# Kernel tuning notes

Hardware: AMD Instinct MI355X
Metric: run time of the kernel (lower is better)

The kernel has to match this reference:

```python
import jax, jax.numpy as jnp
import numpy as np
from jax import lax

B, T, S, J, D = 8, 512, 32, 64, 400
R, MDU, TAGS = 256, 100, 7


def _lstm(x, Wih, Whh, bih, bhh):
    """PyTorch-convention LSTM over x [N,L,Din]; gate order i,f,g,o.
    Returns (hs, cs) each [N,L,R] in scan order (not re-flipped)."""
    N = x.shape[0]
    Rh = Whh.shape[1]
    h0 = jnp.zeros((N, Rh), x.dtype)
    xW = x @ Wih.T + (bih + bhh)  # precompute input projection [N,L,4R]

    def step(carry, xt):
        h, c = carry
        g = xt + h @ Whh.T
        i, f, gg, o = jnp.split(g, 4, axis=-1)
        c = jax.nn.sigmoid(f) * c + jax.nn.sigmoid(i) * jnp.tanh(gg)
        h = jax.nn.sigmoid(o) * jnp.tanh(c)
        return (h, c), (h, c)

    _, (hs, cs) = lax.scan(step, (h0, h0), xW.transpose(1, 0, 2))
    return hs.transpose(1, 0, 2), cs.transpose(1, 0, 2)


def setup_inputs() -> dict:
    key = jax.random.key(0)
    ks = jax.random.split(key, 40)

    def rn(i, shape, s=0.1):
        return s * jax.random.normal(ks[i], shape, jnp.float32)

    inp = {
        'input_text': rn(0, (B, T, D), 1.0),
        'input_syn': rn(1, (B, S, J, D), 1.0),
        'label': jax.random.randint(ks[2], (B, T), 0, TAGS),
        'len_context': jnp.full((B,), T, jnp.int32),
        'len_synopsis': jnp.full((B, S), J, jnp.int32),
    }
    # 6 LSTM parameter sets: context f1/b1 (in=D), synopsis f/b (in=D), modeling f/b (in=4R)
    idx = 3
    for name, din in [('f1', D), ('b1', D), ('sf', D), ('sb', D), ('mf', 4 * R), ('mb', 4 * R)]:
        inp['Wih_' + name] = rn(idx, (4 * R, din)); idx += 1
        inp['Whh_' + name] = rn(idx, (4 * R, R)); idx += 1
        inp['bih_' + name] = rn(idx, (4 * R,)); idx += 1
        inp['bhh_' + name] = rn(idx, (4 * R,)); idx += 1
    inp['W_cWh'] = rn(idx, (MDU, 2 * R)); idx += 1
    inp['W_cWu'] = rn(idx, (MDU, 2 * R)); idx += 1
    inp['W_v'] = rn(idx, (1, MDU)); idx += 1
    inp['W_sWh'] = rn(idx, (2 * R, 2 * R)); idx += 1
    inp['W_sWu'] = rn(idx, (2 * R, 2 * R)); idx += 1
    inp['W_Ws'] = rn(idx, (MDU, 2 * R)); idx += 1
    inp['W_out'] = rn(idx, (TAGS, 6 * R)); idx += 1
    inp['b_out'] = rn(idx, (TAGS,)); idx += 1
    return inp


def reference(input_text, input_syn, label, len_context, len_synopsis,
              Wih_f1, Whh_f1, bih_f1, bhh_f1,
              Wih_b1, Whh_b1, bih_b1, bhh_b1,
              Wih_sf, Whh_sf, bih_sf, bhh_sf,
              Wih_sb, Whh_sb, bih_sb, bhh_sb,
              Wih_mf, Whh_mf, bih_mf, bhh_mf,
              Wih_mb, Whh_mb, bih_mb, bhh_mb,
              W_cWh, W_cWu, W_v, W_sWh, W_sWu, W_Ws, W_out, b_out):
    B_, T_, D_ = input_text.shape
    S_, J_ = input_syn.shape[1], input_syn.shape[2]

    mask = (jnp.arange(T_)[None, :] < len_context[:, None]).astype(input_text.dtype)

    # --- representation layer: manual bi-LSTMCell; backward hiddens kept in scan order ---
    hs_f, cs_f = _lstm(input_text, Wih_f1, Whh_f1, bih_f1, bhh_f1)
    hs_b, cs_b = _lstm(input_text[:, ::-1], Wih_b1, Whh_b1, bih_b1, bhh_b1)
    H = jnp.concatenate([hs_f, hs_b], -1) * mask[..., None]   # [B,T,2R]
    m = jnp.concatenate([cs_f, cs_b], -1) * mask[..., None]   # [B,T,2R]
    x_init = jnp.zeros((B_, 1, 2 * R), input_text.dtype)
    H_full = jnp.concatenate([x_init, H], 1)                  # H_ : [B,T+1,2R]

    # --- synopsis encoder: bi-LSTM final hidden per synopsis sentence ---
    syn = input_syn.reshape(B_ * S_, J_, D_)
    sh_f, _ = _lstm(syn, Wih_sf, Whh_sf, bih_sf, bhh_sf)
    sh_b, _ = _lstm(syn[:, ::-1], Wih_sb, Whh_sb, bih_sb, bhh_sb)
    U = jnp.concatenate([sh_f[:, -1], sh_b[:, -1]], -1).reshape(B_, S_, 2 * R)

    # --- 'ff' co-attention ---
    cWh = H @ W_cWh.T                                          # [B,T,MDU]
    cWu = U @ W_cWu.T                                          # [B,S,MDU]
    z = jnp.tanh(cWh[:, :, None, :] + cWu[:, None, :, :]) @ W_v[0]  # [B,T,S]
    alpha = jax.nn.softmax(z, axis=-1)
    c = jnp.einsum('bts,bsd->btd', alpha, U)                   # [B,T,2R]

    # --- sentinel (ATT_SYN) ---
    Hprev = H_full[:, :T_]                                     # shifted: x_init, H[0..T-2]
    e = jax.nn.sigmoid(Hprev @ W_sWh.T + Hprev @ W_sWu.T)
    s = e * jnp.tanh(m)                                        # [B,T,2R]
    z_hat = jnp.tanh(s @ W_Ws.T + cWh) @ W_v[0]                # [B,T]
    alpha_hat = jax.nn.softmax(jnp.concatenate([z, z_hat[..., None]], -1), axis=-1)
    beta = alpha_hat[:, :, S_:S_ + 1]                          # [B,T,1]
    c_hat = beta * s + (1.0 - beta) * c
    G = jnp.concatenate([H, c_hat], -1)                        # [B,T,4R]

    # --- modeling bi-LSTM (standard aligned outputs) + output projection ---
    mh_f, _ = _lstm(G, Wih_mf, Whh_mf, bih_mf, bhh_mf)
    mh_b, _ = _lstm(G[:, ::-1], Wih_mb, Whh_mb, bih_mb, bhh_mb)
    M = jnp.concatenate([mh_f, mh_b[:, ::-1]], -1)             # [B,T,2R]

    logit = jnp.concatenate([G, M], -1) @ W_out.T + b_out      # [B,T,TAGS]
    return logit
```

## Files before the change

### kernel.cpp

```cpp
#include <hip/hip_runtime.h>
#include <math.h>
#include <stddef.h>


#define BB 8
#define TT 512
#define SS 32
#define JJ 64
#define DD 400
#define RR 256
#define G4 1024
#define H2 512
#define MDU_ 100
#define TAGS_ 7
#define BT (BB*TT)
#define NSEQ (BB*SS)
#define SCH 64
#define MB1 (1024*1024)

typedef __attribute__((ext_vector_type(8))) short short8;
typedef __attribute__((ext_vector_type(4))) float floatx4;
typedef __attribute__((ext_vector_type(4))) unsigned int u32x4;
typedef unsigned short u16;
typedef unsigned int u32;

__device__ __forceinline__ float us2f(u16 u) {
    unsigned int v = ((unsigned int)u) << 16;
    return __builtin_bit_cast(float, v);
}
__device__ __forceinline__ u16 f2us(float f) {
    unsigned int v = __builtin_bit_cast(unsigned int, f);
    v += 0x7FFFu + ((v >> 16) & 1u);
    return (u16)(v >> 16);
}
__device__ __forceinline__ float ldin(const void* p, long i, int bf) {
    return bf ? us2f(((const u16*)p)[i]) : ((const float*)p)[i];
}
__device__ __forceinline__ float sigm(float x) { return 1.0f / (1.0f + expf(-x)); }
__device__ __forceinline__ float sigm_f(float x) { return 1.0f / (1.0f + __expf(-x)); }
__device__ __forceinline__ float tanh_f(float x) {
    float e = __expf(-2.0f * fabsf(x));
    float t = (1.0f - e) / (1.0f + e);
    return copysignf(t, x);
}

__global__ void detect_k(const void* x, int* flag) {
    __shared__ int cnt;
    if (threadIdx.x == 0) cnt = 0;
    __syncthreads();
    u16 lo = ((const u16*)x)[threadIdx.x * 2];
    int e = (lo >> 7) & 0xFF;
    if (e >= 118 && e <= 131) atomicAdd(&cnt, 1);
    __syncthreads();
    if (threadIdx.x == 0) *flag = (cnt > 128) ? 1 : 0;
}
__global__ void castbf_k(const void* src, long off, u16* dst, long n, const int* flag) {
    long i = (long)blockIdx.x * 256 + threadIdx.x;
    if (i < n) dst[i] = (*flag) ? ((const u16*)src)[off + i] : f2us(((const float*)src)[off + i]);
}
__global__ void castf_k(const void* src, float* dst, long n, const int* flag) {
    long i = (long)blockIdx.x * 256 + threadIdx.x;
    if (i < n) dst[i] = ldin(src, i, *flag);
}
__global__ void zero_k(u32* p, long n) {
    long i = (long)blockIdx.x * 256 + threadIdx.x;
    if (i < n) p[i] = 0u;
}
__global__ void bias_sum_k(const void* bih, const void* bhh, float* out, const int* flag) {
    int i = blockIdx.x * 256 + threadIdx.x;
    if (i < G4) out[i] = ldin(bih, i, *flag) + ldin(bhh, i, *flag);
}
__global__ void wsum_k(const void* a, const void* b, u16* o, const int* flag) {
    int i = blockIdx.x * 256 + threadIdx.x;
    if (i < H2 * H2) o[i] = f2us(ldin(a, i, *flag) + ldin(b, i, *flag));
}
__global__ void whh_frag_k(const void* Whh, u16* WF, const int* flag) {
    int i = blockIdx.x * 256 + threadIdx.x;
    if (i >= 4 * 4 * 4 * 8 * 64 * 8) return;
    int j  = i & 7;
    int ln = (i >> 3) & 63;
    int c  = (i >> 9) & 7;
    int t  = (i >> 12) & 3;
    int w  = (i >> 14) & 3;
    int s  = (i >> 16) & 3;
    int n_g = w * 256 + s * 64 + t * 16 + (ln & 15);
    int k   = c * 32 + (ln >> 4) * 8 + j;
    WF[i] = f2us(ldin(Whh, (long)n_g * 256 + k, *flag));
}

#define BM 128
#define BN 128
#define BK 32
#define LDT 40

__global__ __launch_bounds__(256)
void gemm_bt(const u16* __restrict__ A, int lda,
             const u16* __restrict__ W, int ldw,
             void* __restrict__ C, int ldc,
             const float* __restrict__ bias,
             int M, int N, int K, int outBf16)
{
    __shared__ alignas(16) short As[BM * LDT];
    __shared__ alignas(16) short Bs[BN * LDT];
    const int tid  = threadIdx.x;
    const int m0   = blockIdx.y * BM;
    const int n0   = blockIdx.x * BN;
    const int lane = tid & 63;
    const int wave = tid >> 6;
    const int wm   = wave >> 1, wn = wave & 1;
    const int quad = lane >> 4, mrow = lane & 15;

    floatx4 acc[4][4];
#pragma unroll
    for (int i = 0; i < 4; ++i)
#pragma unroll
        for (int j = 0; j < 4; ++j) { floatx4 z4 = {0.f,0.f,0.f,0.f}; acc[i][j] = z4; }

    for (int k0 = 0; k0 < K; k0 += BK) {
#pragma unroll
        for (int cc = 0; cc < 2; ++cc) {
            int c   = tid + cc * 256;
            int row = c >> 2;
            int kc  = (c & 3) << 3;
            int gk  = k0 + kc;
            {
                int gr = m0 + row;
                short8 v;
                if (gr < M && gk + 8 <= K) {
                    v = *(const short8*)(A + (size_t)gr * lda + gk);
                } else {
#pragma unroll
                    for (int e = 0; e < 8; ++e)
                        v[e] = (gr < M && (gk + e) < K) ? (short)A[(size_t)gr * lda + gk + e] : (short)0;
                }
                *(short8*)&As[row * LDT + kc] = v;
            }
            {
                int gn = n0 + row;
                short8 v;
                if (gn < N && gk + 8 <= K) {
                    v = *(const short8*)(W + (size_t)gn * ldw + gk);
                } else {
#pragma unroll
                    for (int e = 0; e < 8; ++e)
                        v[e] = (gn < N && (gk + e) < K) ? (short)W[(size_t)gn * ldw + gk + e] : (short)0;
                }
                *(short8*)&Bs[row * LDT + kc] = v;
            }
        }
        __syncthreads();

        short8 af[4], bf[4];
#pragma unroll
        for (int i = 0; i < 4; ++i)
            af[i] = *(const short8*)&As[(wm * 64 + i * 16 + mrow) * LDT + quad * 8];
#pragma unroll
        for (int j = 0; j < 4; ++j)
            bf[j] = *(const short8*)&Bs[(wn * 64 + j * 16 + mrow) * LDT + quad * 8];
#pragma unroll
        for (int i = 0; i < 4; ++i)
#pragma unroll
            for (int j = 0; j < 4; ++j)
                acc[i][j] = __builtin_amdgcn_mfma_f32_16x16x32_bf16(af[i], bf[j], acc[i][j], 0, 0, 0);
        __syncthreads();
    }

#pragma unroll
    for (int i = 0; i < 4; ++i)
#pragma unroll
        for (int j = 0; j < 4; ++j)
#pragma unroll
            for (int r = 0; r < 4; ++r) {
                int row = m0 + wm * 64 + i * 16 + quad * 4 + r;
                int col = n0 + wn * 64 + j * 16 + mrow;
                if (row < M && col < N) {
                    float v = acc[i][j][r];
                    if (bias) v += bias[col];
                    if (outBf16) ((u16*)C)[(size_t)row * ldc + col] = f2us(v);
                    else         ((float*)C)[(size_t)row * ldc + col] = v;
                }
            }
}

__global__ __launch_bounds__(256, 1)
void lstm_coop(const u16* __restrict__ xWf, const u16* __restrict__ xWb,
               const u16* __restrict__ WFf, const u16* __restrict__ WFb,
               int L,
               u16* __restrict__ hOut, int hStride,
               u16* __restrict__ cOut, int cStride,
               const int* __restrict__ lenp,
               int writeAtSource, int lastOnly, int seqBase,
               u32* __restrict__ hx32, u32* __restrict__ flags,
               int grpBase, int nb, int G8)
{
    const int wgid = blockIdx.x;
    const int s    = wgid / G8;
    const int g    = wgid - s * G8;
    if (g >= 2 * nb) return;
    const int dir  = g / nb;
    const int bat  = g - dir * nb;
    const int tid = threadIdx.x;
    const int wv  = tid >> 6;
    const int ln  = tid & 63;
    const int q   = ln >> 4, m = ln & 15;
    const u16* xW = dir ? xWb : xWf;
    const u16* WF = dir ? WFb : WFf;
    const int grp = grpBase + g;
    u32* flg = flags + (size_t)grp * 64;
    u32* hx  = hx32 + (size_t)grp * 2048;

    __shared__ float g_s[4 * 8 * 64];

    short8 bw[4][8];
    {
        const u16* wb = WF + ((size_t)(s * 4 + wv) * 32) * 512 + ln * 8;
#pragma unroll
        for (int t4 = 0; t4 < 4; ++t4)
#pragma unroll
            for (int c = 0; c < 8; ++c)
                bw[t4][c] = *(const short8*)(wb + (size_t)(t4 * 8 + c) * 512);
    }

    const int seqU = tid >> 5;
    const int j0   = (tid & 31) * 2;
    const int gcol = s * 64 + j0;
    const int mylen = lenp ? lenp[bat * 8 + seqU] : 0x7fffffff;
    float cR0 = 0.f, cR1 = 0.f;

    u32 px0, px1, px2, px3;
    {
        const int tt0 = dir ? (L - 1) : 0;
        const u16* xr = xW + (((size_t)(bat * 8 + seqU)) * L + tt0) * G4 + gcol;
        px0 = *(const u32*)xr;
        px1 = *(const u32*)(xr + 256);
        px2 = *(const u32*)(xr + 512);
        px3 = *(const u32*)(xr + 768);
    }

    for (int t = 0; t < L; ++t) {
        const int tt = dir ? (L - 1 - t) : t;
        short8 a[8];
        if (t > 0) {
            const u32* hp = hx + ((t - 1) & 1) * 1024 + m * 128;
#pragma unroll
            for (int c = 0; c < 8; ++c) {
                if (m < 8) {
                    u32x4 v = *(const u32x4*)(hp + c * 16 + q * 4);
                    a[c] = __builtin_bit_cast(short8, v);
                } else {
                    short8 z = {0,0,0,0,0,0,0,0}; a[c] = z;
                }
            }
        } else {
            short8 z = {0,0,0,0,0,0,0,0};
#pragma unroll
            for (int c = 0; c < 8; ++c) a[c] = z;
        }
        floatx4 acc[4];
#pragma unroll
        for (int t4 = 0; t4 < 4; ++t4) { floatx4 z4 = {0.f,0.f,0.f,0.f}; acc[t4] = z4; }
#pragma unroll
        for (int c = 0; c < 8; ++c)
#pragma unroll
            for (int t4 = 0; t4 < 4; ++t4)
                acc[t4] = __builtin_amdgcn_mfma_f32_16x16x32_bf16(a[c], bw[t4][c], acc[t4], 0, 0, 0);
        if (q < 2) {
#pragma unroll
            for (int t4 = 0; t4 < 4; ++t4)
#pragma unroll
                for (int r = 0; r < 4; ++r)
                    g_s[(wv * 8 + q * 4 + r) * 64 + t4 * 16 + m] = acc[t4][r];
        }
        __syncthreads();
        float hn0, hn1, cn0, cn1;
        {
            float i0 = g_s[(0 * 8 + seqU) * 64 + j0]     + us2f((u16)(px0 & 0xffffu));
            float i1 = g_s[(0 * 8 + seqU) * 64 + j0 + 1] + us2f((u16)(px0 >> 16));
            float f0 = g_s[(1 * 8 + seqU) * 64 + j0]     + us2f((u16)(px1 & 0xffffu));
            float f1 = g_s[(1 * 8 + seqU) * 64 + j0 + 1] + us2f((u16)(px1 >> 16));
            float g0 = g_s[(2 * 8 + seqU) * 64 + j0]     + us2f((u16)(px2 & 0xffffu));
            float g1 = g_s[(2 * 8 + seqU) * 64 + j0 + 1] + us2f((u16)(px2 >> 16));
            float o0 = g_s[(3 * 8 + seqU) * 64 + j0]     + us2f((u16)(px3 & 0xffffu));
            float o1 = g_s[(3 * 8 + seqU) * 64 + j0 + 1] + us2f((u16)(px3 >> 16));
            cn0 = sigm_f(f0) * cR0 + sigm_f(i0) * tanh_f(g0);
            cn1 = sigm_f(f1) * cR1 + sigm_f(i1) * tanh_f(g1);
            hn0 = sigm_f(o0) * tanh_f(cn0);
            hn1 = sigm_f(o1) * tanh_f(cn1);
            cR0 = cn0;
            cR1 = cn1;
            u32 hpack = (u32)f2us(hn0) | ((u32)f2us(hn1) << 16);
            __hip_atomic_store(hx + (t & 1) * 1024 + seqU * 128 + (gcol >> 1),
                               hpack, __ATOMIC_RELAXED, __HIP_MEMORY_SCOPE_AGENT);
        }
        asm volatile("s_waitcnt vmcnt(0)" ::: "memory");
        __syncthreads();
        const bool last = (t == L - 1);
        if (tid == 0 && !last)
            __hip_atomic_store(&flg[s * 16], (u32)(t + 1),
                               __ATOMIC_RELEASE, __HIP_MEMORY_SCOPE_AGENT);
        if (!lastOnly) {
            int wr = writeAtSource ? tt : t;
            float mk = (wr >= mylen) ? 0.f : 1.f;
            size_t ro = ((size_t)(bat * 8 + seqU)) * L + wr;
            u32 hp2 = (u32)f2us(hn0 * mk) | ((u32)f2us(hn1 * mk) << 16);
            *(u32*)(hOut + ro * hStride + dir * RR + gcol) = hp2;
            if (cOut) {
                u32 cp2 = (u32)f2us(cn0 * mk) | ((u32)f2us(cn1 * mk) << 16);
                *(u32*)(cOut + ro * cStride + dir * RR + gcol) = cp2;
            }
        } else if (last) {
            size_t ro = (size_t)(seqBase + bat * 8 + seqU);
            u32 hp2 = (u32)f2us(hn0) | ((u32)f2us(hn1) << 16);
            *(u32*)(hOut + ro * hStride + dir * RR + gcol) = hp2;
        }
        if (!last) {
            {
                const int tn = dir ? (L - 2 - t) : (t + 1);
                const u16* xr = xW + (((size_t)(bat * 8 + seqU)) * L + tn) * G4 + gcol;
                px0 = *(const u32*)xr;
                px1 = *(const u32*)(xr + 256);
                px2 = *(const u32*)(xr + 512);
                px3 = *(const u32*)(xr + 768);
            }
            if (tid == 0) {
                const u32 tgt = (u32)(t + 1);
                long guard = 0;
                for (;;) {
                    u32 f0 = __hip_atomic_load(&flg[0],  __ATOMIC_RELAXED, __HIP_MEMORY_SCOPE_AGENT);
                    u32 f1 = __hip_atomic_load(&flg[16], __ATOMIC_RELAXED, __HIP_MEMORY_SCOPE_AGENT);
                    u32 f2 = __hip_atomic_load(&flg[32], __ATOMIC_RELAXED, __HIP_MEMORY_SCOPE_AGENT);
                    u32 f3 = __hip_atomic_load(&flg[48], __ATOMIC_RELAXED, __HIP_MEMORY_SCOPE_AGENT);
                    if (f0 >= tgt && f1 >= tgt && f2 >= tgt && f3 >= tgt) break;
                    if (++guard > (1L << 18)) break;
                    if (guard > 32) __builtin_amdgcn_s_sleep(1);
                }
                __builtin_amdgcn_fence(__ATOMIC_ACQUIRE, "agent");
            }
            __syncthreads();
        }
    }
}

__global__ void hprev_k(const u16* __restrict__ G, u16* __restrict__ Hp) {
    int idx = blockIdx.x * 256 + threadIdx.x;
    if (idx < BT * H2) {
        int r = idx >> 9, d = idx & 511;
        int t = r & (TT - 1);
        Hp[idx] = (t == 0) ? (u16)0 : G[(size_t)(r - 1) * G4 + d];
    }
}
__global__ void s_k(const float* __restrict__ e, const u16* __restrict__ mB,
                    u16* __restrict__ sB) {
    int i = blockIdx.x * 256 + threadIdx.x;
    if (i < BT * H2) sB[i] = f2us(sigm(e[i]) * tanhf(us2f(mB[i])));
}
__global__ void z_k(const float* __restrict__ cWh, const float* __restrict__ cWu,
                    const float* __restrict__ Wv, float* __restrict__ z) {
    int idx = blockIdx.x * 256 + threadIdx.x;
    if (idx >= BT * SS) return;
    int r = idx >> 5, s = idx & 31;
    int b = r >> 9;
    const float* ph = cWh + (size_t)r * MDU_;
    const float* pu = cWu + (size_t)(b * SS + s) * MDU_;
    float acc = 0.f;
    for (int j = 0; j < MDU_; ++j) acc += tanhf(ph[j] + pu[j]) * Wv[j];
    z[idx] = acc;
}
__global__ void zhat_k(const float* __restrict__ sW, const float* __restrict__ cWh,
                       const float* __restrict__ Wv, float* __restrict__ zhat) {
    int r = blockIdx.x * 256 + threadIdx.x;
    if (r >= BT) return;
    float acc = 0.f;
    const float* ps = sW + (size_t)r * MDU_;
    const float* ph = cWh + (size_t)r * MDU_;
    for (int j = 0; j < MDU_; ++j) acc += tanhf(ps[j] + ph[j]) * Wv[j];
    zhat[r] = acc;
}
__global__ __launch_bounds__(64)
void attn_mix_k(const float* __restrict__ z, const float* __restrict__ zhat,
                const u16* __restrict__ U, const u16* __restrict__ sB,
                u16* __restrict__ G) {
    int r = blockIdx.x;
    int lane = threadIdx.x;
    int b = r >> 9;
    __shared__ float alpha[SS];
    float zv = (lane < SS) ? z[(size_t)r * SS + lane] : -1e30f;
    float mx = zv;
    for (int o = 32; o > 0; o >>= 1) mx = fmaxf(mx, __shfl_xor(mx, o));
    float ez = (lane < SS) ? expf(zv - mx) : 0.f;
    float s1 = ez;
    for (int o = 32; o > 0; o >>= 1) s1 += __shfl_xor(s1, o);
    float zh = zhat[r];
    float mx2 = fmaxf(mx, zh);
    float denom = s1 * expf(mx - mx2) + expf(zh - mx2);
    float beta = expf(zh - mx2) / denom;
    if (lane < SS) alpha[lane] = ez / s1;
    __syncthreads();
    for (int d = lane; d < H2; d += 64) {
        float cv = 0.f;
#pragma unroll 8
        for (int s2 = 0; s2 < SS; ++s2)
            cv += alpha[s2] * us2f(U[(size_t)(b * SS + s2) * H2 + d]);
        float sv = us2f(sB[(size_t)r * H2 + d]);
        G[(size_t)r * G4 + H2 + d] = f2us(beta * sv + (1.f - beta) * cv);
    }
}
__global__ __launch_bounds__(256)
void logit_k(const u16* __restrict__ G, const u16* __restrict__ Mb,
             const u16* __restrict__ Wout, const float* __restrict__ boutF,
             void* __restrict__ out, const int* __restrict__ flag) {
    int r = blockIdx.x * 4 + (threadIdx.x >> 6);
    if (r >= BT) return;
    int lane = threadIdx.x & 63;
    float acc[TAGS_] = {0, 0, 0, 0, 0, 0, 0};
    for (int k = lane; k < 1536; k += 64) {
        float v = (k < G4) ? us2f(G[(size_t)r * G4 + k]) : us2f(Mb[(size_t)r * H2 + (k - G4)]);
#pragma unroll
        for (int tg = 0; tg < TAGS_; ++tg) acc[tg] += v * us2f(Wout[tg * 1536 + k]);
    }
#pragma unroll
    for (int tg = 0; tg < TAGS_; ++tg) {
        float s = acc[tg];
        for (int o = 32; o > 0; o >>= 1) s += __shfl_xor(s, o);
        acc[tg] = s;
    }
    if (lane == 0) {
        int bf = *flag;
#pragma unroll
        for (int tg = 0; tg < TAGS_; ++tg) {
            float v = acc[tg] + boutF[tg];
            if (bf) ((u16*)out)[(size_t)r * TAGS_ + tg] = f2us(v);
            else    ((float*)out)[(size_t)r * TAGS_ + tg] = v;
        }
    }
}

extern "C" void kernel_launch(void* const* d_in, const int* in_sizes, int n_in,
                              void* d_out, int out_size, void* d_ws, size_t ws_size,
                              hipStream_t stream)
{
    const void* x_text = d_in[0];
    const void* x_syn  = d_in[1];
    const int* len_ctx = (const int*)d_in[3];
    const void *Wih[6], *Whh[6], *bih[6], *bhh[6];
    for (int l = 0; l < 6; ++l) {
        Wih[l] = d_in[5 + l * 4 + 0];
        Whh[l] = d_in[5 + l * 4 + 1];
        bih[l] = d_in[5 + l * 4 + 2];
        bhh[l] = d_in[5 + l * 4 + 3];
    }
    const void* W_cWh = d_in[29];
    const void* W_cWu = d_in[30];
    const void* W_v   = d_in[31];
    const void* W_sWh = d_in[32];
    const void* W_sWu = d_in[33];
    const void* W_Ws  = d_in[34];
    const void* W_out = d_in[35];
    const void* b_out = d_in[36];
    (void)in_sizes; (void)n_in; (void)out_size;

    char* ws = (char*)d_ws;
    size_t off = 0;
    auto alloc = [&](size_t bytes) -> void* {
        void* p = ws + off;
        off += (bytes + 255) & ~(size_t)255;
        return p;
    };
    int*   flagB  = (int*)alloc(256);
    float* bsum[6];
    for (int l = 0; l < 6; ++l) bsum[l] = (float*)alloc((size_t)G4 * 4);
    u16*   WsumB  = (u16*)alloc((size_t)H2 * H2 * 2);
    u16*   Ub     = (u16*)alloc((size_t)NSEQ * H2 * 2);
    u16*   Gb     = (u16*)alloc((size_t)BT * G4 * 2);
    u16*   mMb    = (u16*)alloc((size_t)BT * H2 * 2);
    float* cWhB   = (float*)alloc((size_t)BT * MDU_ * 4);
    float* cWuB   = (float*)alloc((size_t)NSEQ * MDU_ * 4);
    float* sWB    = (float*)alloc((size_t)BT * MDU_ * 4);
    float* zB     = (float*)alloc((size_t)BT * SS * 4);
    float* zhatB  = (float*)alloc((size_t)BT * 4);
    u16*   Wcwh16 = (u16*)alloc((size_t)MDU_ * H2 * 2);
    u16*   Wcwu16 = (u16*)alloc((size_t)MDU_ * H2 * 2);
    u16*   Wws16  = (u16*)alloc((size_t)MDU_ * H2 * 2);
    u16*   Wout16 = (u16*)alloc((size_t)TAGS_ * 1536 * 2);
    float* WvF    = (float*)alloc((size_t)MDU_ * 4);
    float* boutF  = (float*)alloc((size_t)TAGS_ * 4);
    u16*   WF[6];
    for (int l = 0; l < 6; ++l) WF[l] = (u16*)alloc((size_t)G4 * RR * 2);
    u32*   cnts   = (u32*)alloc((size_t)128 * 64 * 4);
    u32*   hx32   = (u32*)alloc((size_t)128 * 2048 * 4);

    size_t fixedEnd = off;
    bool bigws = (ws_size >= fixedEnd + (size_t)81 * MB1);
    char* BIG = (char*)alloc(bigws ? (size_t)80 * MB1 : (size_t)24 * MB1);

    u16*   bufA  = (u16*)BIG;
    u16*   bufB  = (u16*)(BIG + (size_t)8 * MB1);
    u16*   x16   = (u16*)(BIG + (size_t)16 * MB1);
    u16*   W16a  = (u16*)(BIG + (size_t)19 * MB1 + MB1 / 2);
    u16*   W16b  = (u16*)(BIG + (size_t)20 * MB1 + MB1 / 2);
    u16*   HprevB = (u16*)BIG;
    float* eBuf   = (float*)(BIG + (size_t)4 * MB1);
    u16*   sBuf   = (u16*)(BIG + (size_t)12 * MB1);
    u16*   mxWf  = (u16*)BIG;
    u16*   mxWb  = (u16*)(BIG + (size_t)8 * MB1);
    u16*   W16aD = (u16*)(BIG + (size_t)16 * MB1);
    u16*   W16bD = (u16*)(BIG + (size_t)18 * MB1);
    u16*   mbufA = (u16*)BIG;
    u16*   mbufB = (u16*)(BIG + (size_t)32 * MB1);
    u16*   mx16  = (u16*)(BIG + (size_t)64 * MB1);
    u16*   mW16a = (u16*)(BIG + (size_t)78 * MB1);
    u16*   mW16b = (u16*)(BIG + (size_t)79 * MB1);

    auto cgrid = [](long n) { return dim3((unsigned)((n + 255) / 256)); };

    detect_k<<<dim3(1), dim3(256), 0, stream>>>(x_text, flagB);
    zero_k<<<cgrid(128 * 64), dim3(256), 0, stream>>>(cnts, 128 * 64);
    castbf_k<<<cgrid(MDU_ * H2), dim3(256), 0, stream>>>(W_cWh, 0, Wcwh16, MDU_ * H2, flagB);
    castbf_k<<<cgrid(MDU_ * H2), dim3(256), 0, stream>>>(W_cWu, 0, Wcwu16, MDU_ * H2, flagB);
    castbf_k<<<cgrid(MDU_ * H2), dim3(256), 0, stream>>>(W_Ws, 0, Wws16, MDU_ * H2, flagB);
    castbf_k<<<cgrid(TAGS_ * 1536), dim3(256), 0, stream>>>(W_out, 0, Wout16, TAGS_ * 1536, flagB);
    castf_k<<<cgrid(MDU_), dim3(256), 0, stream>>>(W_v, WvF, MDU_, flagB);
    castf_k<<<cgrid(TAGS_), dim3(256), 0, stream>>>(b_out, boutF, TAGS_, flagB);
    for (int l = 0; l < 6; ++l) {
        bias_sum_k<<<dim3(4), dim3(256), 0, stream>>>(bih[l], bhh[l], bsum[l], flagB);
        whh_frag_k<<<dim3(1024), dim3(256), 0, stream>>>(Whh[l], WF[l], flagB);
    }
    wsum_k<<<cgrid(H2 * H2), dim3(256), 0, stream>>>(W_sWh, W_sWu, WsumB, flagB);

    if (bigws) {
        castbf_k<<<cgrid(G4 * DD), dim3(256), 0, stream>>>(Wih[2], 0, mW16a, G4 * DD, flagB);
        castbf_k<<<cgrid(G4 * DD), dim3(256), 0, stream>>>(Wih[3], 0, mW16b, G4 * DD, flagB);
        castbf_k<<<cgrid((long)NSEQ * JJ * DD), dim3(256), 0, stream>>>(x_syn, 0, mx16, (long)NSEQ * JJ * DD, flagB);
        gemm_bt<<<dim3(8, (NSEQ * JJ) / BM), dim3(256), 0, stream>>>(mx16, DD, mW16a, DD, mbufA, G4, bsum[2], NSEQ * JJ, G4, DD, 1);
        gemm_bt<<<dim3(8, (NSEQ * JJ) / BM), dim3(256), 0, stream>>>(mx16, DD, mW16b, DD, mbufB, G4, bsum[3], NSEQ * JJ, G4, DD, 1);
        lstm_coop<<<dim3(256), dim3(256), 0, stream>>>(
            mbufA, mbufB, WF[2], WF[3], JJ,
            Ub, H2, (u16*)nullptr, 0, (const int*)nullptr,
            0, 1, 0, hx32, cnts, 4, 32, 64);
    } else {
        castbf_k<<<cgrid(G4 * DD), dim3(256), 0, stream>>>(Wih[2], 0, W16a, G4 * DD, flagB);
        castbf_k<<<cgrid(G4 * DD), dim3(256), 0, stream>>>(Wih[3], 0, W16b, G4 * DD, flagB);
        for (int c = 0; c < NSEQ / SCH; ++c) {
            long chunkElems = (long)SCH * JJ * DD;
            castbf_k<<<cgrid(chunkElems), dim3(256), 0, stream>>>(x_syn, (long)c * chunkElems, x16, chunkElems, flagB);
            gemm_bt<<<dim3(8, (SCH * JJ) / BM), dim3(256), 0, stream>>>(x16, DD, W16a, DD, bufA, G4, bsum[2], SCH * JJ, G4, DD, 1);
            gemm_bt<<<dim3(8, (SCH * JJ) / BM), dim3(256), 0, stream>>>(x16, DD, W16b, DD, bufB, G4, bsum[3], SCH * JJ, G4, DD, 1);
            lstm_coop<<<dim3(64), dim3(256), 0, stream>>>(
                bufA, bufB, WF[2], WF[3], JJ,
                Ub, H2, (u16*)nullptr, 0, (const int*)nullptr,
                0, 1, c * SCH, hx32, cnts, 4 + c * 16, 8, 16);
        }
    }

    castbf_k<<<cgrid((long)BT * DD), dim3(256), 0, stream>>>(x_text, 0, x16, (long)BT * DD, flagB);
    castbf_k<<<cgrid(G4 * DD), dim3(256), 0, stream>>>(Wih[0], 0, W16a, G4 * DD, flagB);
    castbf_k<<<cgrid(G4 * DD), dim3(256), 0, stream>>>(Wih[1], 0, W16b, G4 * DD, flagB);
    gemm_bt<<<dim3(8, 32), dim3(256), 0, stream>>>(x16, DD, W16a, DD, bufA, G4, bsum[0], BT, G4, DD, 1);
    gemm_bt<<<dim3(8, 32), dim3(256), 0, stream>>>(x16, DD, W16b, DD, bufB, G4, bsum[1], BT, G4, DD, 1);
    lstm_coop<<<dim3(32), dim3(256), 0, stream>>>(
        bufA, bufB, WF[0], WF[1], TT,
        Gb, G4, mMb, H2, len_ctx, 0, 0, 0, hx32, cnts, 0, 1, 8);

    gemm_bt<<<dim3(1, 32), dim3(256), 0, stream>>>(Gb, G4, Wcwh16, H2, cWhB, MDU_, nullptr, BT, MDU_, H2, 0);
    gemm_bt<<<dim3(1, 2),  dim3(256), 0, stream>>>(Ub, H2, Wcwu16, H2, cWuB, MDU_, nullptr, NSEQ, MDU_, H2, 0);
    hprev_k<<<cgrid(BT * H2), dim3(256), 0, stream>>>(Gb, HprevB);
    gemm_bt<<<dim3(4, 32), dim3(256), 0, stream>>>(HprevB, H2, WsumB, H2, eBuf, H2, nullptr, BT, H2, H2, 0);
    s_k<<<cgrid(BT * H2), dim3(256), 0, stream>>>(eBuf, mMb, sBuf);
    gemm_bt<<<dim3(1, 32), dim3(256), 0, stream>>>(sBuf, H2, Wws16, H2, sWB, MDU_, nullptr, BT, MDU_, H2, 0);
    z_k<<<cgrid(BT * SS), dim3(256), 0, stream>>>(cWhB, cWuB, WvF, zB);
    zhat_k<<<cgrid(BT), dim3(256), 0, stream>>>(sWB, cWhB, WvF, zhatB);
    attn_mix_k<<<dim3(BT), dim3(64), 0, stream>>>(zB, zhatB, Ub, sBuf, Gb);

    castbf_k<<<cgrid(G4 * G4), dim3(256), 0, stream>>>(Wih[4], 0, W16aD, G4 * G4, flagB);
    castbf_k<<<cgrid(G4 * G4), dim3(256), 0, stream>>>(Wih[5], 0, W16bD, G4 * G4, flagB);
    gemm_bt<<<dim3(8, 32), dim3(256), 0, stream>>>(Gb, G4, W16aD, G4, mxWf, G4, bsum[4], BT, G4, G4, 1);
    gemm_bt<<<dim3(8, 32), dim3(256), 0, stream>>>(Gb, G4, W16bD, G4, mxWb, G4, bsum[5], BT, G4, G4, 1);
    lstm_coop<<<dim3(32), dim3(256), 0, stream>>>(
        mxWf, mxWb, WF[4], WF[5], TT,
        mMb, H2, (u16*)nullptr, 0, (const int*)nullptr, 1, 0, 0, hx32, cnts, 2, 1, 8);

    logit_k<<<dim3(BT / 4), dim3(256), 0, stream>>>(Gb, mMb, Wout16, boutF, d_out, flagB);
}
```

Before: 4.183 ms.

## Co-launch context and synopsis LSTMs in one persistent kernel, overlap output stores with spin-wait

Merges the context bi-LSTM and the synopsis bi-LSTM into a single cooperative launch, with each workgroup choosing its task from its index. The short synopsis recurrence can then run beside the long context recurrence instead of before it. Launch bounds move to 2 blocks per CU so the larger grid stays co-resident, and the context input-projection GEMMs now run before that launch using aliased buffers. The per-step output stores and the next-step x prefetch are split so waves 1-3 issue them before the barrier and wave 0 issues them after the flag wait, hiding them behind synchronisation. The risks are register pressure from the new occupancy bound and correctness problems if the aliased buffers overlap data still in use.

```diff
diff --git a/kernel.cpp b/kernel.cpp
--- a/kernel.cpp
+++ b/kernel.cpp
@@ -182,30 +182,48 @@
             }
 }
 
-__global__ __launch_bounds__(256, 1)
-void lstm_coop(const u16* __restrict__ xWf, const u16* __restrict__ xWb,
-               const u16* __restrict__ WFf, const u16* __restrict__ WFb,
-               int L,
-               u16* __restrict__ hOut, int hStride,
-               u16* __restrict__ cOut, int cStride,
-               const int* __restrict__ lenp,
-               int writeAtSource, int lastOnly, int seqBase,
-               u32* __restrict__ hx32, u32* __restrict__ flags,
-               int grpBase, int nb, int G8)
+__global__ __launch_bounds__(256, 2)
+void lstm_coop(
+    const u16* __restrict__ axWf, const u16* __restrict__ axWb,
+    const u16* __restrict__ aWFf, const u16* __restrict__ aWFb,
+    int aL, u16* __restrict__ ahOut, int ahStride,
+    u16* __restrict__ acOut, int acStride,
+    const int* __restrict__ alenp, int awas, int agrpBase, int anb,
+    const u16* __restrict__ bxWf, const u16* __restrict__ bxWb,
+    const u16* __restrict__ bWFf, const u16* __restrict__ bWFb,
+    int bL, u16* __restrict__ bhOut, int bhStride,
+    int bseqBase, int bgrpBase, int bnb, int boff,
+    u32* __restrict__ hx32, u32* __restrict__ flags, int G8)
 {
     const int wgid = blockIdx.x;
     const int s    = wgid / G8;
     const int g    = wgid - s * G8;
-    if (g >= 2 * nb) return;
-    const int dir  = g / nb;
-    const int bat  = g - dir * nb;
+    const u16 *xW, *WF;
+    u16 *hOut, *cOut;
+    const int* lenp;
+    int L, hStride, cStride, was, lastOnly, seqBase, grp, dir, bat;
+    if (g < 2 * anb) {
+        dir = g / anb; bat = g - dir * anb;
+        xW = dir ? axWb : axWf; WF = dir ? aWFb : aWFf;
+        L = aL; hOut = ahOut; hStride = ahStride;
+        cOut = acOut; cStride = acStride;
+        lenp = alenp; was = awas; lastOnly = 0; seqBase = 0;
+        grp = agrpBase + g;
+    } else if (g >= boff && g < boff + 2 * bnb) {
+        int gb = g - boff;
+        dir = gb / bnb; bat = gb - dir * bnb;
+        xW = dir ? bxWb : bxWf; WF = dir ? bWFb : bWFf;
+        L = bL; hOut = bhOut; hStride = bhStride;
+        cOut = nullptr; cStride = 0;
+        lenp = nullptr; was = 0; lastOnly = 1; seqBase = bseqBase;
+        grp = bgrpBase + gb;
+    } else {
+        return;
+    }
     const int tid = threadIdx.x;
     const int wv  = tid >> 6;
     const int ln  = tid & 63;
     const int q   = ln >> 4, m = ln & 15;
-    const u16* xW = dir ? xWb : xWf;
-    const u16* WF = dir ? WFb : WFf;
-    const int grp = grpBase + g;
     u32* flg = flags + (size_t)grp * 64;
     u32* hx  = hx32 + (size_t)grp * 2048;
 
@@ -236,6 +254,33 @@
         px2 = *(const u32*)(xr + 512);
         px3 = *(const u32*)(xr + 768);
     }
+
+#define DO_OUT() do {                                                         \
+        if (!lastOnly) {                                                      \
+            int wr = was ? tt : t;                                            \
+            float mk = (wr >= mylen) ? 0.f : 1.f;                             \
+            size_t ro = ((size_t)(bat * 8 + seqU)) * L + wr;                  \
+            u32 hp2 = (u32)f2us(hn0 * mk) | ((u32)f2us(hn1 * mk) << 16);      \
+            *(u32*)(hOut + ro * hStride + dir * RR + gcol) = hp2;             \
+            if (cOut) {                                                       \
+                u32 cp2 = (u32)f2us(cn0 * mk) | ((u32)f2us(cn1 * mk) << 16);  \
+                *(u32*)(cOut + ro * cStride + dir * RR + gcol) = cp2;         \
+            }                                                                 \
+        } else if (last) {                                                    \
+            size_t ro = (size_t)(seqBase + bat * 8 + seqU);                   \
+            u32 hp2 = (u32)f2us(hn0) | ((u32)f2us(hn1) << 16);                \
+            *(u32*)(hOut + ro * hStride + dir * RR + gcol) = hp2;             \
+        }                                                                     \
+    } while (0)
+
+#define DO_PREF() do {                                                        \
+        const int tn = dir ? (L - 2 - t) : (t + 1);                           \
+        const u16* xr = xW + (((size_t)(bat * 8 + seqU)) * L + tn) * G4 + gcol; \
+        px0 = *(const u32*)xr;                                                \
+        px1 = *(const u32*)(xr + 256);                                        \
+        px2 = *(const u32*)(xr + 512);                                        \
+        px3 = *(const u32*)(xr + 768);                                        \
+    } while (0)
 
     for (int t = 0; t < L; ++t) {
         const int tt = dir ? (L - 1 - t) : t;
@@ -298,30 +343,8 @@
         if (tid == 0 && !last)
             __hip_atomic_store(&flg[s * 16], (u32)(t + 1),
                                __ATOMIC_RELEASE, __HIP_MEMORY_SCOPE_AGENT);
-        if (!lastOnly) {
-            int wr = writeAtSource ? tt : t;
-            float mk = (wr >= mylen) ? 0.f : 1.f;
-            size_t ro = ((size_t)(bat * 8 + seqU)) * L + wr;
-            u32 hp2 = (u32)f2us(hn0 * mk) | ((u32)f2us(hn1 * mk) << 16);
-            *(u32*)(hOut + ro * hStride + dir * RR + gcol) = hp2;
-            if (cOut) {
-                u32 cp2 = (u32)f2us(cn0 * mk) | ((u32)f2us(cn1 * mk) << 16);
-                *(u32*)(cOut + ro * cStride + dir * RR + gcol) = cp2;
-            }
-        } else if (last) {
-            size_t ro = (size_t)(seqBase + bat * 8 + seqU);
-            u32 hp2 = (u32)f2us(hn0) | ((u32)f2us(hn1) << 16);
-            *(u32*)(hOut + ro * hStride + dir * RR + gcol) = hp2;
-        }
         if (!last) {
-            {
-                const int tn = dir ? (L - 2 - t) : (t + 1);
-                const u16* xr = xW + (((size_t)(bat * 8 + seqU)) * L + tn) * G4 + gcol;
-                px0 = *(const u32*)xr;
-                px1 = *(const u32*)(xr + 256);
-                px2 = *(const u32*)(xr + 512);
-                px3 = *(const u32*)(xr + 768);
-            }
+            if (wv != 0) { DO_OUT(); DO_PREF(); }
             if (tid == 0) {
                 const u32 tgt = (u32)(t + 1);
                 long guard = 0;
@@ -337,8 +360,13 @@
                 __builtin_amdgcn_fence(__ATOMIC_ACQUIRE, "agent");
             }
             __syncthreads();
+            if (wv == 0) { DO_OUT(); DO_PREF(); }
+        } else {
+            DO_OUT();
         }
     }
+#undef DO_OUT
+#undef DO_PREF
 }
 
 __global__ void hprev_k(const u16* __restrict__ G, u16* __restrict__ Hp) {
@@ -510,6 +538,11 @@
     u16*   mx16  = (u16*)(BIG + (size_t)64 * MB1);
     u16*   mW16a = (u16*)(BIG + (size_t)78 * MB1);
     u16*   mW16b = (u16*)(BIG + (size_t)79 * MB1);
+    u16*   bufAc = (u16*)(BIG + (size_t)64 * MB1);
+    u16*   bufBc = (u16*)(BIG + (size_t)72 * MB1);
+    u16*   x16c  = Gb;
+    u16*   W16ac = mMb;
+    u16*   W16bc = mMb + (size_t)G4 * DD;
 
     auto cgrid = [](long n) { return dim3((unsigned)((n + 255) / 256)); };
 
@@ -533,10 +566,15 @@
         castbf_k<<<cgrid((long)NSEQ * JJ * DD), dim3(256), 0, stream>>>(x_syn, 0, mx16, (long)NSEQ * JJ * DD, flagB);
         gemm_bt<<<dim3(8, (NSEQ * JJ) / BM), dim3(256), 0, stream>>>(mx16, DD, mW16a, DD, mbufA, G4, bsum[2], NSEQ * JJ, G4, DD, 1);
         gemm_bt<<<dim3(8, (NSEQ * JJ) / BM), dim3(256), 0, stream>>>(mx16, DD, mW16b, DD, mbufB, G4, bsum[3], NSEQ * JJ, G4, DD, 1);
-        lstm_coop<<<dim3(256), dim3(256), 0, stream>>>(
-            mbufA, mbufB, WF[2], WF[3], JJ,
-            Ub, H2, (u16*)nullptr, 0, (const int*)nullptr,
-            0, 1, 0, hx32, cnts, 4, 32, 64);
+        castbf_k<<<cgrid((long)BT * DD), dim3(256), 0, stream>>>(x_text, 0, x16c, (long)BT * DD, flagB);
+        castbf_k<<<cgrid(G4 * DD), dim3(256), 0, stream>>>(Wih[0], 0, W16ac, G4 * DD, flagB);
+        castbf_k<<<cgrid(G4 * DD), dim3(256), 0, stream>>>(Wih[1], 0, W16bc, G4 * DD, flagB);
+        gemm_bt<<<dim3(8, 32), dim3(256), 0, stream>>>(x16c, DD, W16ac, DD, bufAc, G4, bsum[0], BT, G4, DD, 1);
+        gemm_bt<<<dim3(8, 32), dim3(256), 0, stream>>>(x16c, DD, W16bc, DD, bufBc, G4, bsum[1], BT, G4, DD, 1);
+        lstm_coop<<<dim3(4 * 72), dim3(256), 0, stream>>>(
+            bufAc, bufBc, WF[0], WF[1], TT, Gb, G4, mMb, H2, len_ctx, 0, 0, 1,
+            mbufA, mbufB, WF[2], WF[3], JJ, Ub, H2, 0, 4, 32, 8,
+            hx32, cnts, 72);
     } else {
         castbf_k<<<cgrid(G4 * DD), dim3(256), 0, stream>>>(Wih[2], 0, W16a, G4 * DD, flagB);
         castbf_k<<<cgrid(G4 * DD), dim3(256), 0, stream>>>(Wih[3], 0, W16b, G4 * DD, flagB);
@@ -546,20 +584,22 @@
             gemm_bt<<<dim3(8, (SCH * JJ) / BM), dim3(256), 0, stream>>>(x16, DD, W16a, DD, bufA, G4, bsum[2], SCH * JJ, G4, DD, 1);
             gemm_bt<<<dim3(8, (SCH * JJ) / BM), dim3(256), 0, stream>>>(x16, DD, W16b, DD, bufB, G4, bsum[3], SCH * JJ, G4, DD, 1);
             lstm_coop<<<dim3(64), dim3(256), 0, stream>>>(
-                bufA, bufB, WF[2], WF[3], JJ,
-                Ub, H2, (u16*)nullptr, 0, (const int*)nullptr,
-                0, 1, c * SCH, hx32, cnts, 4 + c * 16, 8, 16);
+                (const u16*)nullptr, (const u16*)nullptr, (const u16*)nullptr, (const u16*)nullptr,
+                0, (u16*)nullptr, 0, (u16*)nullptr, 0, (const int*)nullptr, 0, 0, 0,
+                bufA, bufB, WF[2], WF[3], JJ, Ub, H2, c * SCH, 4 + c * 16, 8, 0,
+                hx32, cnts, 16);
         }
-    }
-
-    castbf_k<<<cgrid((long)BT * DD), dim3(256), 0, stream>>>(x_text, 0, x16, (long)BT * DD, flagB);
-    castbf_k<<<cgrid(G4 * DD), dim3(256), 0, stream>>>(Wih[0], 0, W16a, G4 * DD, flagB);
-    castbf_k<<<cgrid(G4 * DD), dim3(256), 0, stream>>>(Wih[1], 0, W16b, G4 * DD, flagB);
-    gemm_bt<<<dim3(8, 32), dim3(256), 0, stream>>>(x16, DD, W16a, DD, bufA, G4, bsum[0], BT, G4, DD, 1);
-    gemm_bt<<<dim3(8, 32), dim3(256), 0, stream>>>(x16, DD, W16b, DD, bufB, G4, bsum[1], BT, G4, DD, 1);
-    lstm_coop<<<dim3(32), dim3(256), 0, stream>>>(
-        bufA, bufB, WF[0], WF[1], TT,
-        Gb, G4, mMb, H2, len_ctx, 0, 0, 0, hx32, cnts, 0, 1, 8);
+        castbf_k<<<cgrid((long)BT * DD), dim3(256), 0, stream>>>(x_text, 0, x16, (long)BT * DD, flagB);
+        castbf_k<<<cgrid(G4 * DD), dim3(256), 0, stream>>>(Wih[0], 0, W16a, G4 * DD, flagB);
+        castbf_k<<<cgrid(G4 * DD), dim3(256), 0, stream>>>(Wih[1], 0, W16b, G4 * DD, flagB);
+        gemm_bt<<<dim3(8, 32), dim3(256), 0, stream>>>(x16, DD, W16a, DD, bufA, G4, bsum[0], BT, G4, DD, 1);
+        gemm_bt<<<dim3(8, 32), dim3(256), 0, stream>>>(x16, DD, W16b, DD, bufB, G4, bsum[1], BT, G4, DD, 1);
+        lstm_coop<<<dim3(32), dim3(256), 0, stream>>>(
+            bufA, bufB, WF[0], WF[1], TT, Gb, G4, mMb, H2, len_ctx, 0, 0, 1,
+            (const u16*)nullptr, (const u16*)nullptr, (const u16*)nullptr, (const u16*)nullptr,
+            0, (u16*)nullptr, 0, 0, 0, 0, 0,
+            hx32, cnts, 8);
+    }
 
     gemm_bt<<<dim3(1, 32), dim3(256), 0, stream>>>(Gb, G4, Wcwh16, H2, cWhB, MDU_, nullptr, BT, MDU_, H2, 0);
     gemm_bt<<<dim3(1, 2),  dim3(256), 0, stream>>>(Ub, H2, Wcwu16, H2, cWuB, MDU_, nullptr, NSEQ, MDU_, H2, 0);
@@ -576,8 +616,10 @@
     gemm_bt<<<dim3(8, 32), dim3(256), 0, stream>>>(Gb, G4, W16aD, G4, mxWf, G4, bsum[4], BT, G4, G4, 1);
     gemm_bt<<<dim3(8, 32), dim3(256), 0, stream>>>(Gb, G4, W16bD, G4, mxWb, G4, bsum[5], BT, G4, G4, 1);
     lstm_coop<<<dim3(32), dim3(256), 0, stream>>>(
-        mxWf, mxWb, WF[4], WF[5], TT,
-        mMb, H2, (u16*)nullptr, 0, (const int*)nullptr, 1, 0, 0, hx32, cnts, 2, 1, 8);
+        mxWf, mxWb, WF[4], WF[5], TT, mMb, H2, (u16*)nullptr, 0, (const int*)nullptr, 1, 2, 1,
+        (const u16*)nullptr, (const u16*)nullptr, (const u16*)nullptr, (const u16*)nullptr,
+        0, (u16*)nullptr, 0, 0, 0, 0, 0,
+        hx32, cnts, 8);
 
     logit_k<<<dim3(BT / 4), dim3(256), 0, stream>>>(Gb, mMb, Wout16, boutF, d_out, flagB);
 }
```

After: 4.306 ms. 1.03x slower.
